# Performance work log

Hardware: AMD Instinct MI355X
Metric: run time of the kernel (lower is better)

Reference implementation:

```python
import jax, jax.numpy as jnp
import numpy as np

N, L, D = 8192, 50, 64          # batch nodes, history length, embed_dim
NUM_ITEMS, NUM_ATTRS, NUM_FAM = 50000, 100000, 100000


def setup_inputs() -> dict:
    key = jax.random.key(0)
    ks = jax.random.split(key, 12)
    scale = 0.05
    return {
        "nodes": jax.random.randint(ks[0], (N,), 0, NUM_ITEMS),
        "history_va": jax.random.randint(ks[1], (N, L), 0, NUM_ATTRS),
        "history_af": jax.random.randint(ks[2], (N, L), 0, NUM_FAM),
        "v2e_w": jax.random.normal(ks[3], (NUM_ITEMS, D), jnp.float32) * scale,
        "a2e_w": jax.random.normal(ks[4], (NUM_ATTRS, D), jnp.float32) * scale,
        "f2e_w": jax.random.normal(ks[5], (NUM_FAM, D), jnp.float32) * scale,
        "W1": jax.random.normal(ks[6], (3 * D, D), jnp.float32) * scale,
        "b1": jnp.zeros((D,), jnp.float32),
        "W2": jax.random.normal(ks[7], (D, D), jnp.float32) * scale,
        "b2": jnp.zeros((D,), jnp.float32),
        "w3": jax.random.normal(ks[8], (D, 1), jnp.float32) * scale,
        "b3": jnp.zeros((1,), jnp.float32),
    }


def reference(nodes, history_va, history_af, v2e_w, a2e_w, f2e_w,
              W1, b1, W2, b2, w3, b3):
    # Batched form of the per-node loop (va=True branch).
    e_va = a2e_w[history_va]                       # [N, L, D] gathered attr embeds
    e_af = f2e_w[history_af]                       # [N, L, D] gathered famous embeds
    va_rep = v2e_w[nodes]                          # [N, D]    target item embed
    rep = jnp.broadcast_to(va_rep[:, None, :], e_va.shape)
    x = jnp.concatenate([e_va, rep, e_af], axis=-1)  # [N, L, 3D]
    h = jax.nn.relu(x @ W1 + b1)                   # [N, L, D]
    h = jax.nn.relu(h @ W2 + b2)                   # [N, L, D]
    scores = (h @ w3 + b3)[..., 0]                 # [N, L]
    att = jax.nn.softmax(scores, axis=1)           # softmax over history dim
    # e_va.T @ att per node  ==  weighted sum over history
    return jnp.einsum("nld,nl->nd", e_va, att)     # [N, D]
```

## Files before the change

kernel.cpp:

```cpp
#include <hip/hip_runtime.h>
#include <hip/hip_bf16.h>

typedef __bf16    bf16x8 __attribute__((ext_vector_type(8)));
typedef __bf16    bf16x4 __attribute__((ext_vector_type(4)));
typedef _Float16  f16x8  __attribute__((ext_vector_type(8)));
typedef _Float16  f16x4  __attribute__((ext_vector_type(4)));
typedef float     f32x4  __attribute__((ext_vector_type(4)));

#define HL 50
#define DD 64


__global__ __launch_bounds__(256, 4) void prep_all_kernel(
    const int*   __restrict__ nodes,
    const float* __restrict__ v2e,
    const float* __restrict__ a2e,
    const float* __restrict__ f2e,
    const float* __restrict__ W1,
    const float* __restrict__ b1,
    const float* __restrict__ W2,
    const float* __restrict__ b2,
    const float* __restrict__ w3,
    _Float16* __restrict__ A2, _Float16* __restrict__ F2,
    _Float16* __restrict__ E16, _Float16* __restrict__ ba16,
    _Float16* __restrict__ w2f, float* __restrict__ wsc,
    int nA, int nF, int N, int GA, int GF, int GB)
{
    __shared__ __align__(16) _Float16 es[64 * 72];
    const int tid  = threadIdx.x;
    const int w    = tid >> 6, lane = tid & 63;
    const int lq   = lane & 15, quad = lane >> 4;
    const int col  = w * 16 + lq;
    const int bid  = blockIdx.x;

    if (bid < GA + GF) {
        const bool  isA   = (bid < GA);
        const int   rb    = isA ? bid : bid - GA;
        const int   nrows = isA ? nA : nF;
        const float* src  = isA ? a2e : f2e;
        const float* Wp   = isA ? W1 : (W1 + 128 * DD);
        _Float16*   dst   = isA ? A2 : F2;
        const int   r0    = rb * 64;

        #pragma unroll
        for (int i = 0; i < 4; ++i) {
            int t = i * 256 + tid;
            int row = t >> 4, q = t & 15;
            int gr = r0 + row; if (gr >= nrows) gr = nrows - 1;
            float4 v = *(const float4*)(src + (size_t)gr * DD + q * 4);
            f16x4 pk = {(_Float16)v.x, (_Float16)v.y, (_Float16)v.z, (_Float16)v.w};
            *(f16x4*)&es[row * 72 + q * 4] = pk;
            if (isA) *(f16x4*)(E16 + (size_t)gr * DD + q * 4) = pk;
        }
        f16x8 bfr[2];
        #pragma unroll
        for (int t = 0; t < 2; ++t)
            #pragma unroll
            for (int j = 0; j < 8; ++j)
                bfr[t][j] = (_Float16)Wp[(t * 32 + quad * 8 + j) * DD + col];
        __syncthreads();

        f32x4 acc[4];
        #pragma unroll
        for (int mt = 0; mt < 4; ++mt) acc[mt] = (f32x4){0.f, 0.f, 0.f, 0.f};
        #pragma unroll
        for (int t = 0; t < 2; ++t)
            #pragma unroll
            for (int mt = 0; mt < 4; ++mt) {
                f16x8 a = *(const f16x8*)&es[(mt * 16 + lq) * 72 + t * 32 + quad * 8];
                acc[mt] = __builtin_amdgcn_mfma_f32_16x16x32_f16(a, bfr[t], acc[mt], 0, 0, 0);
            }
        __syncthreads();
        #pragma unroll
        for (int mt = 0; mt < 4; ++mt)
            #pragma unroll
            for (int r = 0; r < 4; ++r)
                es[(mt * 16 + quad * 4 + r) * 72 + col] = (_Float16)acc[mt][r];
        __syncthreads();
        {
            int row = tid >> 2, seg = tid & 3;
            int gr = r0 + row;
            if (gr < nrows) {
                f16x8 vv = *(const f16x8*)&es[row * 72 + seg * 16];
                *(f16x8*)(dst + (size_t)gr * DD + seg * 16) = vv;
            }
        }
    } else if (bid < GA + GF + GB) {
        const int n0 = (bid - GA - GF) * 64;
        #pragma unroll
        for (int i = 0; i < 4; ++i) {
            int t = i * 256 + tid;
            int row = t >> 4, q = t & 15;
            int gn = n0 + row; if (gn >= N) gn = N - 1;
            int idx = nodes[gn];
            float4 v = *(const float4*)(v2e + (size_t)idx * DD + q * 4);
            f16x4 pk = {(_Float16)v.x, (_Float16)v.y, (_Float16)v.z, (_Float16)v.w};
            *(f16x4*)&es[row * 72 + q * 4] = pk;
        }
        f16x8 bfr[2];
        #pragma unroll
        for (int t = 0; t < 2; ++t)
            #pragma unroll
            for (int j = 0; j < 8; ++j)
                bfr[t][j] = (_Float16)W1[(64 + t * 32 + quad * 8 + j) * DD + col];
        const float b1c = b1[col];
        __syncthreads();

        f32x4 acc[4];
        #pragma unroll
        for (int mt = 0; mt < 4; ++mt) acc[mt] = (f32x4){0.f, 0.f, 0.f, 0.f};
        #pragma unroll
        for (int t = 0; t < 2; ++t)
            #pragma unroll
            for (int mt = 0; mt < 4; ++mt) {
                f16x8 a = *(const f16x8*)&es[(mt * 16 + lq) * 72 + t * 32 + quad * 8];
                acc[mt] = __builtin_amdgcn_mfma_f32_16x16x32_f16(a, bfr[t], acc[mt], 0, 0, 0);
            }
        #pragma unroll
        for (int mt = 0; mt < 4; ++mt)
            #pragma unroll
            for (int r = 0; r < 4; ++r) {
                int gn = n0 + mt * 16 + quad * 4 + r;
                if (gn < N) ba16[(size_t)gn * DD + col] = (_Float16)(acc[mt][r] + b1c);
            }
    } else {
        const int ln = tid & 63, c0 = tid >> 6;
        #pragma unroll
        for (int h = 0; h < 2; ++h) {
            int combo = c0 + 4 * h;
            int ct = combo >> 1, t = combo & 1;
            _Float16* d = w2f + ((size_t)combo * 64 + ln) * 8;
            #pragma unroll
            for (int j = 0; j < 8; ++j)
                d[j] = (_Float16)W2[(t * 32 + (ln >> 4) * 8 + j) * DD + ct * 16 + (ln & 15)];
        }
        if (tid < 64) { wsc[tid] = w3[tid]; wsc[64 + tid] = b2[tid]; }
    }
}

__global__ __launch_bounds__(256, 8) void va_main_kernel(
    const int*      __restrict__ hva,
    const int*      __restrict__ haf,
    const _Float16* __restrict__ A2,
    const _Float16* __restrict__ F2,
    const _Float16* __restrict__ E16,
    const _Float16* __restrict__ ba16,
    const _Float16* __restrict__ w2f,
    const float*    __restrict__ wsc,
    float*          __restrict__ out)
{
    __shared__ float pbuf[64];
    __shared__ float ps[4 * 64];

    const int tid  = threadIdx.x;
    const int w    = tid >> 6;
    const int lane = tid & 63;
    const int lq   = lane & 15;
    const int quad = lane >> 4;
    const int node = blockIdx.x;
    const int* hb = hva + node * HL;
    const int* fb = haf + node * HL;

    const int  lr0   = w * 16 + lq;
    const bool valid = (lr0 < HL);
    f16x8 h1f[2];
    #pragma unroll
    for (int t = 0; t < 2; ++t)
        #pragma unroll
        for (int j = 0; j < 8; ++j) h1f[t][j] = (_Float16)0.f;
    if (valid) {
        const int ia  = hb[lr0];
        const int ifm = fb[lr0];
        f16x8 a2g[2], f2g[2], bag[2];
        #pragma unroll
        for (int t = 0; t < 2; ++t) {
            a2g[t] = *(const f16x8*)(A2   + (size_t)ia   * DD + t * 32 + quad * 8);
            f2g[t] = *(const f16x8*)(F2   + (size_t)ifm  * DD + t * 32 + quad * 8);
            bag[t] = *(const f16x8*)(ba16 + (size_t)node * DD + t * 32 + quad * 8);
        }
        #pragma unroll
        for (int t = 0; t < 2; ++t) {
            f16x8 h = a2g[t] + f2g[t] + bag[t];
            #pragma unroll
            for (int j = 0; j < 8; ++j)
                h1f[t][j] = (h[j] > (_Float16)0.f) ? h[j] : (_Float16)0.f;
        }
    }

    float srow[4] = {0.f, 0.f, 0.f, 0.f};
    #pragma unroll
    for (int ct = 0; ct < 4; ++ct) {
        const float b2c = wsc[64 + ct * 16 + lq];
        f32x4 acc = {b2c, b2c, b2c, b2c};
        #pragma unroll
        for (int t = 0; t < 2; ++t) {
            f16x8 bfr = *(const f16x8*)(w2f + ((size_t)(ct * 2 + t) * 64 + lane) * 8);
            acc = __builtin_amdgcn_mfma_f32_16x16x32_f16(h1f[t], bfr, acc, 0, 0, 0);
        }
        const float w3c = wsc[ct * 16 + lq];
        #pragma unroll
        for (int r = 0; r < 4; ++r)
            srow[r] = fmaf(fmaxf(acc[r], 0.f), w3c, srow[r]);
    }
    #pragma unroll
    for (int r = 0; r < 4; ++r) {
        #pragma unroll
        for (int m = 1; m < 16; m <<= 1) srow[r] += __shfl_xor(srow[r], m);
    }
    if (lq == 0) {
        #pragma unroll
        for (int r = 0; r < 4; ++r) pbuf[w * 16 + quad * 4 + r] = srow[r];
    }

    const int iv = hb[(lane < HL) ? lane : 0];
    float ev[13];
    #pragma unroll
    for (int i = 0; i < 13; ++i) {
        int l = w + 4 * i;
        if (l < HL) {
            int idx = __shfl(iv, l);
            ev[i] = (float)E16[(size_t)idx * DD + lane];
        }
    }
    __syncthreads();

    float att;
    {
        float s = (lane < HL) ? pbuf[lane] : -3.0e38f;
        float mx = s;
        #pragma unroll
        for (int m = 1; m < 64; m <<= 1) mx = fmaxf(mx, __shfl_xor(mx, m));
        float e = (lane < HL) ? __expf(s - mx) : 0.f;
        float sm = e;
        #pragma unroll
        for (int m = 1; m < 64; m <<= 1) sm += __shfl_xor(sm, m);
        att = e / sm;
    }

    float o = 0.f;
    #pragma unroll
    for (int i = 0; i < 13; ++i) {
        int l = w + 4 * i;
        if (l < HL) {
            float av = __shfl(att, l);
            o = fmaf(av, ev[i], o);
        }
    }
    ps[w * 64 + lane] = o;
    __syncthreads();
    if (w == 0)
        out[(size_t)node * DD + lane] =
            ps[lane] + ps[64 + lane] + ps[128 + lane] + ps[192 + lane];
}

#define FMR  112
#define FMT  7
#define FXSS 136

__global__ __launch_bounds__(256) void fb_prep_kernel(
    const float* __restrict__ W1, const float* __restrict__ W2,
    const float* __restrict__ w3, const float* __restrict__ b1,
    const float* __restrict__ b2,
    __bf16* __restrict__ wf, float* __restrict__ wsc)
{
    const int tid  = threadIdx.x;
    const int quad = tid >> 6;
    const int col  = tid & 63;
    __bf16* dst = wf + tid * 64;
    #pragma unroll
    for (int t = 0; t < 4; ++t)
        #pragma unroll
        for (int j = 0; j < 8; ++j) {
            int keff = t * 32 + quad * 8 + j;
            int krow = (keff < 64) ? keff : keff + 64;
            dst[t * 8 + j] = (__bf16)W1[krow * 64 + col];
        }
    #pragma unroll
    for (int t = 0; t < 2; ++t)
        #pragma unroll
        for (int j = 0; j < 8; ++j) {
            dst[32 + t * 8 + j] = (__bf16)W1[(64 + t * 32 + quad * 8 + j) * 64 + col];
            dst[48 + t * 8 + j] = (__bf16)W2[(t * 32 + quad * 8 + j) * 64 + col];
        }
    if (tid < 64) {
        wsc[tid] = w3[tid]; wsc[64 + tid] = b1[tid]; wsc[128 + tid] = b2[tid];
    }
}

__global__ __launch_bounds__(256, 5) void fb_agg_kernel(
    const int* __restrict__ nodes, const int* __restrict__ hva,
    const int* __restrict__ haf, const float* __restrict__ v2e,
    const float* __restrict__ a2e, const float* __restrict__ f2e,
    const __bf16* __restrict__ wf, const float* __restrict__ wsc,
    float* __restrict__ out)
{
    __shared__ __bf16 xs[FMR * FXSS];
    __shared__ float  pbuf[4 * FMR];
    const int tid = threadIdx.x;
    const int w = tid >> 6, lane = tid & 63, lq = lane & 15, quad = lane >> 4;
    const int col = w * 16 + lq;
    const int n0 = blockIdx.x * 2;
    {
        const int* hb = hva + n0 * HL;
        const int* fb = haf + n0 * HL;
        #pragma unroll
        for (int i = 0; i < 13; ++i) {
            int t = i * 256 + tid;
            if (t < 2 * HL * 2 * 16) {
                int r = t >> 4, q = t & 15;
                bool va = (r < 2 * HL);
                int gr = va ? r : r - 2 * HL;
                int idx = va ? hb[gr] : fb[gr];
                const float* src = (va ? a2e : f2e) + (size_t)idx * DD + q * 4;
                float4 v = *(const float4*)src;
                bf16x4 pk = {(__bf16)v.x, (__bf16)v.y, (__bf16)v.z, (__bf16)v.w};
                *(bf16x4*)&xs[gr * FXSS + (va ? 0 : DD) + q * 4] = pk;
            }
        }
    }
    bf16x8 repf[2];
    #pragma unroll
    for (int t = 0; t < 2; ++t)
        #pragma unroll
        for (int j = 0; j < 8; ++j) repf[t][j] = (__bf16)0.f;
    if (lq < 2) {
        int nd = nodes[n0 + lq];
        const float* rp = v2e + (size_t)nd * DD;
        #pragma unroll
        for (int t = 0; t < 2; ++t) {
            float4 v0 = *(const float4*)(rp + t * 32 + quad * 8);
            float4 v1 = *(const float4*)(rp + t * 32 + quad * 8 + 4);
            repf[t] = (bf16x8){(__bf16)v0.x, (__bf16)v0.y, (__bf16)v0.z, (__bf16)v0.w,
                               (__bf16)v1.x, (__bf16)v1.y, (__bf16)v1.z, (__bf16)v1.w};
        }
    }
    const __bf16* fbp = wf + (size_t)(quad * 64 + col) * 64;
    bf16x8 b1f[4], b1u[2], b2f[2];
    #pragma unroll
    for (int t = 0; t < 4; ++t) b1f[t] = *(const bf16x8*)(fbp + t * 8);
    #pragma unroll
    for (int t = 0; t < 2; ++t) {
        b1u[t] = *(const bf16x8*)(fbp + 32 + t * 8);
        b2f[t] = *(const bf16x8*)(fbp + 48 + t * 8);
    }
    const float w3c = wsc[col];
    const float b1c = wsc[64 + col];
    const float b2c = wsc[128 + col];
    f32x4 rb = {0.f, 0.f, 0.f, 0.f};
    #pragma unroll
    for (int t = 0; t < 2; ++t)
        rb = __builtin_amdgcn_mfma_f32_16x16x32_bf16(repf[t], b1u[t], rb, 0, 0, 0);
    const float bias0 = __shfl(rb[0], lq) + b1c;
    const float bias1 = __shfl(rb[1], lq) + b1c;
    __syncthreads();
    f32x4 acc[FMT];
    #pragma unroll
    for (int mt = 0; mt < FMT; ++mt)
        #pragma unroll
        for (int r = 0; r < 4; ++r) {
            int gr = mt * 16 + quad * 4 + r;
            acc[mt][r] = (gr >= HL) ? bias1 : bias0;
        }
    #pragma unroll
    for (int t = 0; t < 4; ++t)
        #pragma unroll
        for (int mt = 0; mt < FMT; ++mt) {
            bf16x8 a = *(const bf16x8*)&xs[(mt * 16 + lq) * FXSS + t * 32 + quad * 8];
            acc[mt] = __builtin_amdgcn_mfma_f32_16x16x32_bf16(a, b1f[t], acc[mt], 0, 0, 0);
        }
    __syncthreads();
    #pragma unroll
    for (int mt = 0; mt < FMT; ++mt)
        #pragma unroll
        for (int r = 0; r < 4; ++r) {
            int gr = mt * 16 + quad * 4 + r;
            xs[gr * FXSS + DD + col] = (__bf16)fmaxf(acc[mt][r], 0.f);
        }
    __syncthreads();
    f32x4 a2[FMT];
    #pragma unroll
    for (int mt = 0; mt < FMT; ++mt) a2[mt] = (f32x4){b2c, b2c, b2c, b2c};
    #pragma unroll
    for (int t = 0; t < 2; ++t)
        #pragma unroll
        for (int mt = 0; mt < FMT; ++mt) {
            bf16x8 a = *(const bf16x8*)&xs[(mt * 16 + lq) * FXSS + DD + t * 32 + quad * 8];
            a2[mt] = __builtin_amdgcn_mfma_f32_16x16x32_bf16(a, b2f[t], a2[mt], 0, 0, 0);
        }
    #pragma unroll
    for (int mt = 0; mt < FMT; ++mt) {
        float p0 = fmaxf(a2[mt][0], 0.f) * w3c;
        float p1 = fmaxf(a2[mt][1], 0.f) * w3c;
        float p2 = fmaxf(a2[mt][2], 0.f) * w3c;
        float p3 = fmaxf(a2[mt][3], 0.f) * w3c;
        #pragma unroll
        for (int m = 1; m < 16; m <<= 1) {
            p0 += __shfl_xor(p0, m); p1 += __shfl_xor(p1, m);
            p2 += __shfl_xor(p2, m); p3 += __shfl_xor(p3, m);
        }
        if (lq == 0) {
            int rowb = mt * 16 + quad * 4;
            pbuf[w * FMR + rowb + 0] = p0; pbuf[w * FMR + rowb + 1] = p1;
            pbuf[w * FMR + rowb + 2] = p2; pbuf[w * FMR + rowb + 3] = p3;
        }
    }
    __syncthreads();
    const int n = w & 1, lh = w >> 1;
    float att;
    {
        float s = -3.0e38f;
        if (lane < HL) {
            int gr = n * HL + lane;
            s = pbuf[gr] + pbuf[FMR + gr] + pbuf[2 * FMR + gr] + pbuf[3 * FMR + gr];
        }
        float mx = s;
        #pragma unroll
        for (int m = 1; m < 64; m <<= 1) mx = fmaxf(mx, __shfl_xor(mx, m));
        float e = (lane < HL) ? __expf(s - mx) : 0.f;
        float sm = e;
        #pragma unroll
        for (int m = 1; m < 64; m <<= 1) sm += __shfl_xor(sm, m);
        att = e / sm;
    }
    {
        float o = 0.f;
        const int lb = lh * 25;
        #pragma unroll
        for (int i = 0; i < 25; ++i) {
            int l = lb + i;
            float av = __shfl(att, l);
            o = fmaf(av, (float)xs[(n * HL + l) * FXSS + lane], o);
        }
        float* op = (float*)&xs[(100 + w) * FXSS + DD];
        op[lane] = o;
    }
    __syncthreads();
    if (w < 2) {
        const float* p0 = (const float*)&xs[(100 + w) * FXSS + DD];
        const float* p1 = (const float*)&xs[(100 + w + 2) * FXSS + DD];
        out[(size_t)(n0 + w) * DD + lane] = p0[lane] + p1[lane];
    }
}

extern "C" void kernel_launch(void* const* d_in, const int* in_sizes, int n_in,
                              void* d_out, int out_size, void* d_ws, size_t ws_size,
                              hipStream_t stream) {
    const int*   nodes = (const int*)d_in[0];
    const int*   hva   = (const int*)d_in[1];
    const int*   haf   = (const int*)d_in[2];
    const float* v2e   = (const float*)d_in[3];
    const float* a2e   = (const float*)d_in[4];
    const float* f2e   = (const float*)d_in[5];
    const float* W1    = (const float*)d_in[6];
    const float* b1    = (const float*)d_in[7];
    const float* W2    = (const float*)d_in[8];
    const float* b2    = (const float*)d_in[9];
    const float* w3    = (const float*)d_in[10];
    float* out = (float*)d_out;

    const int N  = in_sizes[0];
    const int nA = in_sizes[4] / DD;
    const int nF = in_sizes[5] / DD;

    size_t offA2 = 0;
    size_t offF2 = (offA2 + (size_t)nA * DD * 2 + 255) & ~(size_t)255;
    size_t offE  = (offF2 + (size_t)nF * DD * 2 + 255) & ~(size_t)255;
    size_t offBA = (offE  + (size_t)nA * DD * 2 + 255) & ~(size_t)255;
    size_t offWF = (offBA + (size_t)N * DD * 2 + 255) & ~(size_t)255;
    size_t offSC = offWF + 8 * 64 * 8 * 2;
    size_t need  = offSC + 128 * 4;

    if (ws_size >= need) {
        _Float16* A2  = (_Float16*)((char*)d_ws + offA2);
        _Float16* F2  = (_Float16*)((char*)d_ws + offF2);
        _Float16* E16 = (_Float16*)((char*)d_ws + offE);
        _Float16* ba  = (_Float16*)((char*)d_ws + offBA);
        _Float16* w2f = (_Float16*)((char*)d_ws + offWF);
        float*    wsc = (float*)((char*)d_ws + offSC);

        const int GA = (nA + 63) / 64;
        const int GF = (nF + 63) / 64;
        const int GB = (N + 63) / 64;
        prep_all_kernel<<<GA + GF + GB + 1, 256, 0, stream>>>(
            nodes, v2e, a2e, f2e, W1, b1, W2, b2, w3,
            A2, F2, E16, ba, w2f, wsc, nA, nF, N, GA, GF, GB);
        va_main_kernel<<<N, 256, 0, stream>>>(hva, haf, A2, F2, E16, ba, w2f, wsc, out);
    } else {
        __bf16* wf  = (__bf16*)d_ws;
        float*  wsc = (float*)((char*)d_ws + 256 * 64 * 2);
        fb_prep_kernel<<<1, 256, 0, stream>>>(W1, W2, w3, b1, b2, wf, wsc);
        fb_agg_kernel<<<N / 2, 256, 0, stream>>>(nodes, hva, haf, v2e, a2e, f2e,
                                                 wf, wsc, out);
    }
}
```

Baseline: 160.0 us.

## Map one node per wavefront instead of one node per block

The main kernel now assigns each wavefront a whole node, and each block handles four nodes. A wave loops over the four 16-row MFMA tiles, gathers the scores through lane shuffles, and does the softmax and weighted sum of E16 rows itself. This removes the shared-memory buffers and both __syncthreads barriers, and cuts the block count by four. In exchange each wave does four times the serial work, holds more registers (occupancy hint lowered from 8 to 6), and the grid assumes N is divisible by 4.

After: 214.1 us. 33.8% more time.

```diff
diff --git a/kernel.cpp b/kernel.cpp
--- a/kernel.cpp
+++ b/kernel.cpp
@@ -138,7 +138,7 @@
     }
 }
 
-__global__ __launch_bounds__(256, 8) void va_main_kernel(
+__global__ __launch_bounds__(256, 6) void va_main_kernel(
     const int*      __restrict__ hva,
     const int*      __restrict__ haf,
     const _Float16* __restrict__ A2,
@@ -149,84 +149,86 @@
     const float*    __restrict__ wsc,
     float*          __restrict__ out)
 {
-    __shared__ float pbuf[64];
-    __shared__ float ps[4 * 64];
-
     const int tid  = threadIdx.x;
     const int w    = tid >> 6;
     const int lane = tid & 63;
     const int lq   = lane & 15;
     const int quad = lane >> 4;
-    const int node = blockIdx.x;
+    const int node = blockIdx.x * 4 + w;
     const int* hb = hva + node * HL;
     const int* fb = haf + node * HL;
 
-    const int  lr0   = w * 16 + lq;
-    const bool valid = (lr0 < HL);
-    f16x8 h1f[2];
+    const int li   = (lane < HL) ? lane : (HL - 1);
+    const int iv_a = hb[li];
+    const int iv_f = fb[li];
+
+    f16x8 bag[2];
     #pragma unroll
     for (int t = 0; t < 2; ++t)
-        #pragma unroll
-        for (int j = 0; j < 8; ++j) h1f[t][j] = (_Float16)0.f;
-    if (valid) {
-        const int ia  = hb[lr0];
-        const int ifm = fb[lr0];
-        f16x8 a2g[2], f2g[2], bag[2];
-        #pragma unroll
-        for (int t = 0; t < 2; ++t) {
-            a2g[t] = *(const f16x8*)(A2   + (size_t)ia   * DD + t * 32 + quad * 8);
-            f2g[t] = *(const f16x8*)(F2   + (size_t)ifm  * DD + t * 32 + quad * 8);
-            bag[t] = *(const f16x8*)(ba16 + (size_t)node * DD + t * 32 + quad * 8);
-        }
-        #pragma unroll
-        for (int t = 0; t < 2; ++t) {
-            f16x8 h = a2g[t] + f2g[t] + bag[t];
-            #pragma unroll
-            for (int j = 0; j < 8; ++j)
-                h1f[t][j] = (h[j] > (_Float16)0.f) ? h[j] : (_Float16)0.f;
-        }
-    }
-
-    float srow[4] = {0.f, 0.f, 0.f, 0.f};
-    #pragma unroll
-    for (int ct = 0; ct < 4; ++ct) {
-        const float b2c = wsc[64 + ct * 16 + lq];
-        f32x4 acc = {b2c, b2c, b2c, b2c};
-        #pragma unroll
-        for (int t = 0; t < 2; ++t) {
-            f16x8 bfr = *(const f16x8*)(w2f + ((size_t)(ct * 2 + t) * 64 + lane) * 8);
-            acc = __builtin_amdgcn_mfma_f32_16x16x32_f16(h1f[t], bfr, acc, 0, 0, 0);
-        }
-        const float w3c = wsc[ct * 16 + lq];
-        #pragma unroll
-        for (int r = 0; r < 4; ++r)
-            srow[r] = fmaf(fmaxf(acc[r], 0.f), w3c, srow[r]);
-    }
-    #pragma unroll
-    for (int r = 0; r < 4; ++r) {
-        #pragma unroll
-        for (int m = 1; m < 16; m <<= 1) srow[r] += __shfl_xor(srow[r], m);
-    }
-    if (lq == 0) {
-        #pragma unroll
-        for (int r = 0; r < 4; ++r) pbuf[w * 16 + quad * 4 + r] = srow[r];
-    }
-
-    const int iv = hb[(lane < HL) ? lane : 0];
-    float ev[13];
-    #pragma unroll
-    for (int i = 0; i < 13; ++i) {
-        int l = w + 4 * i;
-        if (l < HL) {
-            int idx = __shfl(iv, l);
-            ev[i] = (float)E16[(size_t)idx * DD + lane];
-        }
-    }
-    __syncthreads();
+        bag[t] = *(const f16x8*)(ba16 + (size_t)node * DD + t * 32 + quad * 8);
+
+    float sall[16];
+    #pragma unroll
+    for (int mt = 0; mt < 4; ++mt) {
+        const int row = mt * 16 + lq;
+        const bool rv = (row < HL);
+        f16x8 h1f[2];
+        #pragma unroll
+        for (int t = 0; t < 2; ++t)
+            #pragma unroll
+            for (int j = 0; j < 8; ++j) h1f[t][j] = (_Float16)0.f;
+        if (rv) {
+            const int ia  = __shfl(iv_a, row);
+            const int ifm = __shfl(iv_f, row);
+            #pragma unroll
+            for (int t = 0; t < 2; ++t) {
+                f16x8 a2g = *(const f16x8*)(A2 + (size_t)ia  * DD + t * 32 + quad * 8);
+                f16x8 f2g = *(const f16x8*)(F2 + (size_t)ifm * DD + t * 32 + quad * 8);
+                f16x8 h = a2g + f2g + bag[t];
+                #pragma unroll
+                for (int j = 0; j < 8; ++j)
+                    h1f[t][j] = (h[j] > (_Float16)0.f) ? h[j] : (_Float16)0.f;
+            }
+        }
+        float srow[4] = {0.f, 0.f, 0.f, 0.f};
+        #pragma unroll
+        for (int ct = 0; ct < 4; ++ct) {
+            const float b2c = wsc[64 + ct * 16 + lq];
+            f32x4 acc = {b2c, b2c, b2c, b2c};
+            #pragma unroll
+            for (int t = 0; t < 2; ++t) {
+                f16x8 bfr = *(const f16x8*)(w2f + ((size_t)(ct * 2 + t) * 64 + lane) * 8);
+                acc = __builtin_amdgcn_mfma_f32_16x16x32_f16(h1f[t], bfr, acc, 0, 0, 0);
+            }
+            const float w3c = wsc[ct * 16 + lq];
+            #pragma unroll
+            for (int r = 0; r < 4; ++r)
+                srow[r] = fmaf(fmaxf(acc[r], 0.f), w3c, srow[r]);
+        }
+        #pragma unroll
+        for (int r = 0; r < 4; ++r) {
+            #pragma unroll
+            for (int m = 1; m < 16; m <<= 1) srow[r] += __shfl_xor(srow[r], m);
+            sall[mt * 4 + r] = srow[r];
+        }
+    }
+
+    float s = -3.0e38f;
+    {
+        const int srcl = ((lane >> 2) & 3) * 16;
+        const int mymt = lane >> 4, myreg = lane & 3;
+        #pragma unroll
+        for (int mt = 0; mt < 4; ++mt)
+            #pragma unroll
+            for (int reg = 0; reg < 4; ++reg) {
+                float v = __shfl(sall[mt * 4 + reg], srcl);
+                s = (mymt == mt && myreg == reg) ? v : s;
+            }
+        if (lane >= HL) s = -3.0e38f;
+    }
 
     float att;
     {
-        float s = (lane < HL) ? pbuf[lane] : -3.0e38f;
         float mx = s;
         #pragma unroll
         for (int m = 1; m < 64; m <<= 1) mx = fmaxf(mx, __shfl_xor(mx, m));
@@ -237,20 +239,28 @@
         att = e / sm;
     }
 
-    float o = 0.f;
-    #pragma unroll
-    for (int i = 0; i < 13; ++i) {
-        int l = w + 4 * i;
-        if (l < HL) {
-            float av = __shfl(att, l);
-            o = fmaf(av, ev[i], o);
-        }
-    }
-    ps[w * 64 + lane] = o;
-    __syncthreads();
-    if (w == 0)
-        out[(size_t)node * DD + lane] =
-            ps[lane] + ps[64 + lane] + ps[128 + lane] + ps[192 + lane];
+    float o0 = 0.f, o1 = 0.f, o2 = 0.f, o3 = 0.f;
+    #pragma unroll
+    for (int i = 0; i < 48; i += 4) {
+        int i0 = hb[i + 0];
+        int i1 = hb[i + 1];
+        int i2 = hb[i + 2];
+        int i3 = hb[i + 3];
+        float v0 = (float)E16[(size_t)i0 * DD + lane];
+        float v1 = (float)E16[(size_t)i1 * DD + lane];
+        float v2 = (float)E16[(size_t)i2 * DD + lane];
+        float v3 = (float)E16[(size_t)i3 * DD + lane];
+        o0 = fmaf(__shfl(att, i + 0), v0, o0);
+        o1 = fmaf(__shfl(att, i + 1), v1, o1);
+        o2 = fmaf(__shfl(att, i + 2), v2, o2);
+        o3 = fmaf(__shfl(att, i + 3), v3, o3);
+    }
+    {
+        int i0 = hb[48], i1 = hb[49];
+        o0 = fmaf(__shfl(att, 48), (float)E16[(size_t)i0 * DD + lane], o0);
+        o1 = fmaf(__shfl(att, 49), (float)E16[(size_t)i1 * DD + lane], o1);
+    }
+    out[(size_t)node * DD + lane] = (o0 + o1) + (o2 + o3);
 }
 
 #define FMR  112
@@ -484,7 +494,7 @@
         prep_all_kernel<<<GA + GF + GB + 1, 256, 0, stream>>>(
             nodes, v2e, a2e, f2e, W1, b1, W2, b2, w3,
             A2, F2, E16, ba, w2f, wsc, nA, nF, N, GA, GF, GB);
-        va_main_kernel<<<N, 256, 0, stream>>>(hva, haf, A2, F2, E16, ba, w2f, wsc, out);
+        va_main_kernel<<<N / 4, 256, 0, stream>>>(hva, haf, A2, F2, E16, ba, w2f, wsc, out);
     } else {
         __bf16* wf  = (__bf16*)d_ws;
         float*  wsc = (float*)((char*)d_ws + 256 * 64 * 2);
```
